# Kernel tuning notes

Measured on AMD Instinct MI355X. Metric: run time of the kernel, lower is better.

## Reference

```python
import jax, jax.numpy as jnp
import numpy as np

B, H, W, D = 4, 64, 64, 384
M, P = 12, 9
DH = D // M             # 32 head dim
DFF = 3 * D             # 1152 FFN hidden
N = H * W               # 4096 queries (single level)


def setup_inputs():
    key = jax.random.key(0)
    ks = jax.random.split(key, 12)
    g = lambda k, s, sc=0.02: jax.random.normal(k, s, jnp.float32) * sc
    return {
        "x": jax.random.normal(ks[0], (B, D, H, W), jnp.float32),
        "qry_masks": jnp.zeros((B, H, W), jnp.float32),
        "so_w": g(ks[1], (M * P * 2, D)), "so_b": g(ks[2], (M * P * 2,)),
        "aw_w": g(ks[3], (M * P, D)), "aw_b": g(ks[4], (M * P,)),
        "vp_w": g(ks[5], (D, D)), "vp_b": jnp.zeros((D,), jnp.float32),
        "op_w": g(ks[6], (D, D)), "op_b": jnp.zeros((D,), jnp.float32),
        "ln1_g": jnp.ones((D,), jnp.float32), "ln1_b": jnp.zeros((D,), jnp.float32),
        "w1": g(ks[7], (DFF, D)), "w2": g(ks[8], (D, DFF)),
        "ln2_g": jnp.ones((D,), jnp.float32), "ln2_b": jnp.zeros((D,), jnp.float32),
        "level_embed": g(ks[9], (1, D), 1.0),
    }


def _layernorm(x, g, b, eps=1e-5):
    mu = x.mean(-1, keepdims=True)
    v = ((x - mu) ** 2).mean(-1, keepdims=True)
    return (x - mu) * jax.lax.rsqrt(v + eps) * g + b


def _sine_pos(mask):
    # mask: [B,H,W] bool. mmdet SinePositionalEncoding(num_feats=D//2, normalize=True)
    not_mask = (~mask).astype(jnp.float32)
    y = jnp.cumsum(not_mask, 1)
    x = jnp.cumsum(not_mask, 2)
    eps, scale = 1e-6, 2.0 * np.pi
    y = y / (y[:, -1:, :] + eps) * scale
    x = x / (x[:, :, -1:] + eps) * scale
    nf = D // 2
    dim_t = 10000.0 ** (2.0 * (jnp.arange(nf) // 2).astype(jnp.float32) / nf)
    px, py = x[..., None] / dim_t, y[..., None] / dim_t

    def interleave(p):
        return jnp.stack([jnp.sin(p[..., 0::2]), jnp.cos(p[..., 1::2])], -1).reshape(p.shape[:-1] + (nf,))

    return jnp.concatenate([interleave(py), interleave(px)], -1)  # [B,H,W,D]


def _bilinear_gather(v, px, py):
    # v: [B,M,HW,DH]; px,py: [B,M,NP] pixel coords (grid_sample align_corners=False, zero pad)
    x0 = jnp.floor(px); y0 = jnp.floor(py)
    lx, ly = px - x0, py - y0
    x0i, y0i = x0.astype(jnp.int32), y0.astype(jnp.int32)
    out = jnp.zeros(v.shape[:2] + (px.shape[-1], v.shape[-1]), v.dtype)
    for dx, dy, wgt in ((0, 0, (1 - lx) * (1 - ly)), (1, 0, lx * (1 - ly)),
                        (0, 1, (1 - lx) * ly), (1, 1, lx * ly)):
        xi, yi = x0i + dx, y0i + dy
        valid = ((xi >= 0) & (xi < W) & (yi >= 0) & (yi < H)).astype(v.dtype)
        idx = jnp.clip(yi, 0, H - 1) * W + jnp.clip(xi, 0, W - 1)
        g = jnp.take_along_axis(v, idx[..., None], axis=2)  # [B,M,NP,DH]
        out = out + (wgt * valid)[..., None] * g
    return out


def _msdeform_attn(q, value_in, ref, mask_flat,
                   so_w, so_b, aw_w, aw_b, vp_w, vp_b, op_w, op_b):
    value = value_in @ vp_w.T + vp_b                      # [B,N,D]
    value = jnp.where(mask_flat[..., None], 0.0, value)
    so = (q @ so_w.T + so_b).reshape(B, N, M, P, 2)       # single level
    aw = jax.nn.softmax((q @ aw_w.T + aw_b).reshape(B, N, M, P), axis=-1)
    norm = jnp.array([W, H], jnp.float32)
    loc = ref[:, :, None, None, :] + so / norm            # [B,N,M,P,2] in [0,1]
    v = value.reshape(B, N, M, DH).transpose(0, 2, 1, 3)  # [B,M,HW,DH]
    px = (loc[..., 0] * W - 0.5).transpose(0, 2, 1, 3).reshape(B, M, N * P)
    py = (loc[..., 1] * H - 0.5).transpose(0, 2, 1, 3).reshape(B, M, N * P)
    sampled = _bilinear_gather(v, px, py).reshape(B, M, N, P, DH)
    out = jnp.einsum('bmnpd,bnmp->bnmd', sampled, aw).reshape(B, N, D)
    return out @ op_w.T + op_b


def reference(x, qry_masks, so_w, so_b, aw_w, aw_b, vp_w, vp_b, op_w, op_b,
              ln1_g, ln1_b, w1, w2, ln2_g, ln2_b, level_embed):
    mask = (qry_masks == 255.0)                           # [B,H,W] bool
    pos = _sine_pos(mask).reshape(B, N, D) + level_embed[0]
    src = x.reshape(B, D, N).transpose(0, 2, 1)           # [B,N,D]
    mask_flat = mask.reshape(B, N)
    gy, gx = jnp.meshgrid((jnp.arange(H, dtype=jnp.float32) + 0.5) / H,
                          (jnp.arange(W, dtype=jnp.float32) + 0.5) / W, indexing='ij')
    ref = jnp.stack([gx.reshape(-1), gy.reshape(-1)], -1)[None]  # [1,N,2] (x,y)
    q = src
    attn = _msdeform_attn(q + pos, q, ref, mask_flat,
                          so_w, so_b, aw_w, aw_b, vp_w, vp_b, op_w, op_b)
    q = _layernorm(q + attn, ln1_g, ln1_b)
    q = _layernorm(q + jax.nn.relu(q @ w1.T) @ w2.T, ln2_g, ln2_b)
    return q.transpose(0, 2, 1).reshape(B, D, H, W)
```

## Files before the change

kernel.cpp:

```cpp
#include <hip/hip_runtime.h>
#include <math.h>

#define Bc   4
#define Hc   64
#define Wc   64
#define Dc   384
#define Nc   4096
#define Mc   12
#define Pc   9
#define DHc  32
#define DFFc 1152
#define BNc  (Bc*Nc)

typedef __attribute__((ext_vector_type(8))) short short8;
typedef __attribute__((ext_vector_type(4))) float floatx4;

__device__ __forceinline__ ushort f2bf(float f) {
    union { float f; unsigned u; } v; v.f = f;
    unsigned r = v.u + 0x7fffu + ((v.u >> 16) & 1u);
    return (ushort)(r >> 16);
}
__device__ __forceinline__ float bf2f(ushort u) {
    union { unsigned u; float f; } v; v.u = (unsigned)u << 16; return v.f;
}

__device__ __forceinline__ void gload_lds16(const void* g, void* l) {
    __builtin_amdgcn_global_load_lds(
        (const __attribute__((address_space(1))) void*)(uintptr_t)g,
        (__attribute__((address_space(3))) void*)(uintptr_t)l,
        16, 0, 0);
}

#define SOW_N  82944
#define AWW_N  41472
#define VPW_N  147456
#define OPW_N  147456
#define W1_N   442368
#define W2_N   442368
#define WTOT   1304064

__global__ void init_kernel(const float* __restrict__ so_w,
                            const float* __restrict__ aw_w,
                            const float* __restrict__ vp_w,
                            const float* __restrict__ op_w,
                            const float* __restrict__ w1,
                            const float* __restrict__ w2,
                            const float* __restrict__ so_b,
                            const float* __restrict__ aw_b,
                            const float* __restrict__ qmask,
                            ushort* __restrict__ out,
                            float* __restrict__ bias_out,
                            float* __restrict__ cum_y,
                            float* __restrict__ cum_x) {
    int i = blockIdx.x * 256 + threadIdx.x;
    if (i < WTOT) {
        float v;
        int j = i;
        if (j < SOW_N) v = so_w[j];
        else if ((j -= SOW_N) < AWW_N) v = aw_w[j];
        else if ((j -= AWW_N) < VPW_N) v = vp_w[j];
        else if ((j -= VPW_N) < OPW_N) v = op_w[j];
        else if ((j -= OPW_N) < W1_N)  v = w1[j];
        else { j -= W1_N; v = w2[j]; }
        out[i] = f2bf(v);
        return;
    }
    int j = i - WTOT;
    if (j < 384) {
        bias_out[j] = (j < 216) ? so_b[j] : (j < 324 ? aw_b[j - 216] : 0.f);
        return;
    }
    int t = j - 384;
    if (t < Bc * Wc) {
        int b = t / Wc, w = t % Wc;
        float run = 0.f;
        for (int h = 0; h < Hc; ++h) {
            run += (qmask[(b * Hc + h) * Wc + w] == 255.0f) ? 0.f : 1.f;
            cum_y[(b * Hc + h) * Wc + w] = run;
        }
    } else if (t < Bc * Wc + Bc * Hc) {
        int t2 = t - Bc * Wc;
        int b = t2 / Hc, h = t2 % Hc;
        float run = 0.f;
        for (int w = 0; w < Wc; ++w) {
            run += (qmask[(b * Hc + h) * Wc + w] == 255.0f) ? 0.f : 1.f;
            cum_x[(b * Hc + h) * Wc + w] = run;
        }
    }
}

__global__ void transpose_pos_kernel(const float* __restrict__ x,
                                     const float* __restrict__ cum_y,
                                     const float* __restrict__ cum_x,
                                     const float* __restrict__ level_embed,
                                     ushort* __restrict__ src_bf,
                                     ushort* __restrict__ qpos_bf) {
    __shared__ float tile[32][33];
    int b  = blockIdx.z;
    int n0 = blockIdx.x * 32, d0 = blockIdx.y * 32;
    int tx = threadIdx.x, ty = threadIdx.y;
    tile[ty][tx] = x[((size_t)b * Dc + (d0 + ty)) * Nc + (n0 + tx)];
    __syncthreads();
    int n = n0 + ty, d = d0 + tx;
    float v = tile[tx][ty];
    size_t oi = ((size_t)b * Nc + n) * Dc + d;
    src_bf[oi] = f2bf(v);
    int h = n >> 6, w = n & 63;
    const float TWO_PI = 6.28318530717958647692f;
    float vy = cum_y[(b * Hc + h) * Wc + w] /
               (cum_y[(b * Hc + (Hc - 1)) * Wc + w] + 1e-6f) * TWO_PI;
    float vx = cum_x[(b * Hc + h) * Wc + w] /
               (cum_x[(b * Hc + h) * Wc + (Wc - 1)] + 1e-6f) * TWO_PI;
    int   i  = (d < 192) ? d : d - 192;
    float vv = (d < 192) ? vy : vx;
    float e   = (float)(i >> 1) * (2.0f / 192.0f);
    float idt = exp2f(e * -13.28771237954945f);
    float ang = vv * idt;
    float pe  = (i & 1) ? __cosf(ang) : __sinf(ang);
    qpos_bf[oi] = f2bf(v + pe + level_embed[d]);
}

template <int KT>
__device__ __forceinline__ void gemm_core(
        const ushort* __restrict__ A, const ushort* __restrict__ Wt,
        const float* __restrict__ bias,
        float* __restrict__ Cf, ushort* __restrict__ Cb,
        int Nout, int relu, const float* __restrict__ qmask,
        ushort* As, ushort* Bs) {
    constexpr int NCH = KT / 32;
    const int tid  = threadIdx.x;
    const int m0   = blockIdx.x * 128;
    const int n0   = blockIdx.y * 128;
    const int lane = tid & 63;
    const int wv   = tid >> 6;
    const int wr   = (wv >> 1) * 64;
    const int wc   = (wv & 1) * 64;
    const int quad = lane >> 4;
    const int lrow = lane & 15;
    const int srow = wv * 32 + (lane >> 2);
    const int scol = (lane & 3) * 8;

    floatx4 acc[4][4];
    #pragma unroll
    for (int i = 0; i < 4; ++i)
        #pragma unroll
        for (int j = 0; j < 4; ++j)
            acc[i][j] = (floatx4)(0.f);

    #pragma unroll
    for (int s = 0; s < 2; ++s) {
        gload_lds16(A  + (size_t)(m0 + srow + s * 16) * KT + scol,
                    As + wv * 1024 + s * 512);
        gload_lds16(Wt + (size_t)(n0 + srow + s * 16) * KT + scol,
                    Bs + wv * 1024 + s * 512);
    }

    for (int c = 0; c < NCH; ++c) {
        const int cur = c & 1;
        __syncthreads();
        if (c + 1 < NCH) {
            const int k0 = (c + 1) * 32;
            #pragma unroll
            for (int s = 0; s < 2; ++s) {
                gload_lds16(A  + (size_t)(m0 + srow + s * 16) * KT + k0 + scol,
                            As + (cur ^ 1) * 4096 + wv * 1024 + s * 512);
                gload_lds16(Wt + (size_t)(n0 + srow + s * 16) * KT + k0 + scol,
                            Bs + (cur ^ 1) * 4096 + wv * 1024 + s * 512);
            }
        }
        short8 afr[4], bfr[4];
        #pragma unroll
        for (int i = 0; i < 4; ++i)
            afr[i] = *(const short8*)(As + cur * 4096 +
                                      (wr + i * 16 + lrow) * 32 + quad * 8);
        #pragma unroll
        for (int j = 0; j < 4; ++j)
            bfr[j] = *(const short8*)(Bs + cur * 4096 +
                                      (wc + j * 16 + lrow) * 32 + quad * 8);
        #pragma unroll
        for (int i = 0; i < 4; ++i)
            #pragma unroll
            for (int j = 0; j < 4; ++j)
                acc[i][j] = __builtin_amdgcn_mfma_f32_16x16x32_bf16(
                    afr[i], bfr[j], acc[i][j], 0, 0, 0);
    }

    float mz[4][4];
    #pragma unroll
    for (int i = 0; i < 4; ++i)
        #pragma unroll
        for (int r = 0; r < 4; ++r) {
            int row = m0 + wr + i * 16 + quad * 4 + r;
            mz[i][r] = (qmask && qmask[row] == 255.0f) ? 0.f : 1.f;
        }

    #pragma unroll
    for (int i = 0; i < 4; ++i) {
        #pragma unroll
        for (int j = 0; j < 4; ++j) {
            int col = n0 + wc + j * 16 + lrow;
            if (col >= Nout) continue;
            float bsv = bias ? bias[col] : 0.f;
            #pragma unroll
            for (int r = 0; r < 4; ++r) {
                int row = m0 + wr + i * 16 + quad * 4 + r;
                float v = acc[i][j][r] + bsv;
                if (relu) v = fmaxf(v, 0.f);
                v *= mz[i][r];
                if (Cf) Cf[(size_t)row * Nout + col] = v;
                if (Cb) Cb[(size_t)row * Nout + col] = f2bf(v);
            }
        }
    }
}

template <int KT>
__global__ __launch_bounds__(256) void gemm_single_kernel(
        const ushort* __restrict__ A, const ushort* __restrict__ Wt,
        const float* __restrict__ bias,
        float* __restrict__ Cf, ushort* __restrict__ Cb,
        int Nout, int relu, const float* __restrict__ qmask) {
    __shared__ ushort As[2 * 128 * 32];
    __shared__ ushort Bs[2 * 128 * 32];
    gemm_core<KT>(A, Wt, bias, Cf, Cb, Nout, relu, qmask, As, Bs);
}

__global__ __launch_bounds__(256) void gemm_dual_kernel(
        const ushort* __restrict__ A0, const ushort* __restrict__ W0,
        const float* __restrict__ b0, float* __restrict__ Cf0,
        const ushort* __restrict__ A1, const ushort* __restrict__ W1,
        const float* __restrict__ b1, ushort* __restrict__ Cb1,
        const float* __restrict__ qmask) {
    __shared__ ushort As[2 * 128 * 32];
    __shared__ ushort Bs[2 * 128 * 32];
    if (blockIdx.z == 0)
        gemm_core<384>(A0, W0, b0, Cf0, nullptr, 384, 0, nullptr, As, Bs);
    else
        gemm_core<384>(A1, W1, b1, nullptr, Cb1, 384, 0, qmask, As, Bs);
}

template <int KT, int MODE>
__global__ __launch_bounds__(512, 4) void gemm_fullrow_kernel(
        const ushort* __restrict__ A, const ushort* __restrict__ Wt,
        const float* __restrict__ bias, const void* __restrict__ resid,
        const float* __restrict__ g, const float* __restrict__ beta,
        float* __restrict__ outf, ushort* __restrict__ outb) {
    constexpr int NCH = KT / 32;
    __shared__ ushort smem[26624];
    __shared__ float eps1[8][32], eps2[8][32];
    __shared__ float mu_l[32], rs_l[32];
    ushort* As = smem;
    ushort* Bs = smem + 2048;
    const int tid  = threadIdx.x;
    const int lane = tid & 63;
    const int wv   = tid >> 6;
    const int quad = lane >> 4;
    const int lrow = lane & 15;
    const int m0   = blockIdx.x * 32;
    const int srow = lane >> 2;
    const int scol = (lane & 3) * 8;

    floatx4 acc[2][3];
    #pragma unroll
    for (int i = 0; i < 2; ++i)
        #pragma unroll
        for (int j = 0; j < 3; ++j)
            acc[i][j] = (floatx4)(0.f);

    if (wv < 2)
        gload_lds16(A + (size_t)(m0 + wv * 16 + srow) * KT + scol,
                    As + wv * 512);
    #pragma unroll
    for (int s = 0; s < 3; ++s)
        gload_lds16(Wt + (size_t)(wv * 48 + s * 16 + srow) * KT + scol,
                    Bs + wv * 1536 + s * 512);

    for (int c = 0; c < NCH; ++c) {
        const int cur = c & 1;
        __syncthreads();
        if (c + 1 < NCH) {
            const int k0 = (c + 1) * 32;
            if (wv < 2)
                gload_lds16(A + (size_t)(m0 + wv * 16 + srow) * KT + k0 + scol,
                            As + (cur ^ 1) * 1024 + wv * 512);
            #pragma unroll
            for (int s = 0; s < 3; ++s)
                gload_lds16(Wt + (size_t)(wv * 48 + s * 16 + srow) * KT + k0 + scol,
                            Bs + (cur ^ 1) * 12288 + wv * 1536 + s * 512);
        }
        short8 afr[2], bfr[3];
        #pragma unroll
        for (int i = 0; i < 2; ++i)
            afr[i] = *(const short8*)(As + cur * 1024 +
                                      (i * 16 + lrow) * 32 + quad * 8);
        #pragma unroll
        for (int j = 0; j < 3; ++j)
            bfr[j] = *(const short8*)(Bs + cur * 12288 +
                                      (wv * 48 + j * 16 + lrow) * 32 + quad * 8);
        #pragma unroll
        for (int i = 0; i < 2; ++i)
            #pragma unroll
            for (int j = 0; j < 3; ++j)
                acc[i][j] = __builtin_amdgcn_mfma_f32_16x16x32_bf16(
                    afr[i], bfr[j], acc[i][j], 0, 0, 0);
    }

    float s1[8], s2[8];
    #pragma unroll
    for (int k = 0; k < 8; ++k) { s1[k] = 0.f; s2[k] = 0.f; }
    #pragma unroll
    for (int i = 0; i < 2; ++i) {
        #pragma unroll
        for (int r = 0; r < 4; ++r) {
            int rl = i * 16 + quad * 4 + r;
            #pragma unroll
            for (int j = 0; j < 3; ++j) {
                int col = wv * 48 + j * 16 + lrow;
                float t = acc[i][j][r];
                if (bias) t += bias[col];
                if (MODE == 0)
                    t += bf2f(((const ushort*)resid)[(size_t)(m0 + rl) * Dc + col]);
                else
                    t += ((const float*)resid)[(size_t)(m0 + rl) * Dc + col];
                acc[i][j][r] = t;
                s1[i * 4 + r] += t;
                s2[i * 4 + r] += t * t;
            }
        }
    }
    #pragma unroll
    for (int mm = 1; mm < 16; mm <<= 1) {
        #pragma unroll
        for (int k = 0; k < 8; ++k) {
            s1[k] += __shfl_xor(s1[k], mm);
            s2[k] += __shfl_xor(s2[k], mm);
        }
    }
    if (lrow == 0) {
        #pragma unroll
        for (int i = 0; i < 2; ++i)
            #pragma unroll
            for (int r = 0; r < 4; ++r) {
                int rl = i * 16 + quad * 4 + r;
                eps1[wv][rl] = s1[i * 4 + r];
                eps2[wv][rl] = s2[i * 4 + r];
            }
    }
    __syncthreads();
    if (tid < 32) {
        float a1 = 0.f, a2 = 0.f;
        #pragma unroll
        for (int w = 0; w < 8; ++w) { a1 += eps1[w][tid]; a2 += eps2[w][tid]; }
        float mu  = a1 * (1.0f / Dc);
        float var = a2 * (1.0f / Dc) - mu * mu;
        mu_l[tid] = mu;
        rs_l[tid] = rsqrtf(var + 1e-5f);
    }
    __syncthreads();

    #pragma unroll
    for (int i = 0; i < 2; ++i) {
        #pragma unroll
        for (int r = 0; r < 4; ++r) {
            int rl = i * 16 + quad * 4 + r;
            float mu = mu_l[rl], rs = rs_l[rl];
            #pragma unroll
            for (int j = 0; j < 3; ++j) {
                int col = wv * 48 + j * 16 + lrow;
                acc[i][j][r] = (acc[i][j][r] - mu) * rs * g[col] + beta[col];
            }
        }
    }

    if (MODE == 0) {
        #pragma unroll
        for (int i = 0; i < 2; ++i)
            #pragma unroll
            for (int j = 0; j < 3; ++j) {
                int col = wv * 48 + j * 16 + lrow;
                #pragma unroll
                for (int r = 0; r < 4; ++r) {
                    int rl = i * 16 + quad * 4 + r;
                    float v = acc[i][j][r];
                    outf[(size_t)(m0 + rl) * Dc + col] = v;
                    outb[(size_t)(m0 + rl) * Dc + col] = f2bf(v);
                }
            }
    } else {
        float* tile = (float*)smem;
        const int b   = m0 >> 12;
        const int n0r = m0 & 4095;
        #pragma unroll
        for (int gp = 0; gp < 2; ++gp) {
            __syncthreads();
            if ((wv >> 2) == gp) {
                int cbase = (wv & 3) * 48;
                #pragma unroll
                for (int i = 0; i < 2; ++i)
                    #pragma unroll
                    for (int j = 0; j < 3; ++j) {
                        int c = cbase + j * 16 + lrow;
                        #pragma unroll
                        for (int r = 0; r < 4; ++r) {
                            int rl = i * 16 + quad * 4 + r;
                            tile[rl * 193 + c] = acc[i][j][r];
                        }
                    }
            }
            __syncthreads();
            const int row = tid & 31;
            const int cp  = tid >> 5;
            #pragma unroll
            for (int it = 0; it < 12; ++it) {
                int c = it * 16 + cp;
                outf[((size_t)(b * Dc + gp * 192 + c)) * Nc + n0r + row] =
                    tile[row * 193 + c];
            }
        }
    }
}

__global__ __launch_bounds__(256) void deform_attn_kernel(
        const ushort* __restrict__ value_bf, const float* __restrict__ soaw,
        ushort* __restrict__ out) {
    int bid   = blockIdx.x;
    int slice = bid % 48;
    int h     = bid / 48;
    int m  = slice % Mc;
    int b  = slice / Mc;
    int w  = threadIdx.x >> 2;
    int l4 = threadIdx.x & 3;
    int n  = (h << 6) | w;
    int bn = b * Nc + n;
    const float* sop = soaw + (size_t)bn * 384 + m * 18;
    const float* lgt = soaw + (size_t)bn * 384 + 216 + m * Pc;
    float awv[Pc];
    float mx = lgt[0];
    #pragma unroll
    for (int i = 1; i < Pc; ++i) mx = fmaxf(mx, lgt[i]);
    float ssum = 0.f;
    #pragma unroll
    for (int i = 0; i < Pc; ++i) { awv[i] = __expf(lgt[i] - mx); ssum += awv[i]; }
    float sinv = 1.f / ssum;
    const ushort* vb = value_bf + ((size_t)b * Nc) * Dc + m * DHc + l4 * 8;
    float acc[8] = {0.f, 0.f, 0.f, 0.f, 0.f, 0.f, 0.f, 0.f};
    #pragma unroll
    for (int p = 0; p < Pc; ++p) {
        float2 so2 = *(const float2*)(sop + p * 2);
        float px = (float)w + so2.x;
        float py = (float)h + so2.y;
        float x0f = floorf(px), y0f = floorf(py);
        float lx = px - x0f, ly = py - y0f;
        int x0 = (int)x0f, y0 = (int)y0f;
        int x1 = x0 + 1,  y1 = y0 + 1;
        float a = awv[p] * sinv;
        float w00 = (1.f - lx) * (1.f - ly) * a;
        float w01 = lx * (1.f - ly) * a;
        float w10 = (1.f - lx) * ly * a;
        float w11 = lx * ly * a;
        bool bx0 = (unsigned)x0 < 64u, bx1 = (unsigned)x1 < 64u;
        bool by0 = (unsigned)y0 < 64u, by1 = (unsigned)y1 < 64u;
        w00 = (bx0 && by0) ? w00 : 0.f;
        w01 = (bx1 && by0) ? w01 : 0.f;
        w10 = (bx0 && by1) ? w10 : 0.f;
        w11 = (bx1 && by1) ? w11 : 0.f;
        int cx0 = min(max(x0, 0), 63), cx1 = min(max(x1, 0), 63);
        int cy0 = min(max(y0, 0), 63), cy1 = min(max(y1, 0), 63);
        uint4 q00 = *(const uint4*)(vb + (size_t)(cy0 * 64 + cx0) * Dc);
        uint4 q01 = *(const uint4*)(vb + (size_t)(cy0 * 64 + cx1) * Dc);
        uint4 q10 = *(const uint4*)(vb + (size_t)(cy1 * 64 + cx0) * Dc);
        uint4 q11 = *(const uint4*)(vb + (size_t)(cy1 * 64 + cx1) * Dc);
        union { unsigned u; float f; } t;
        #define ACC2(word, wg, k)                                   \
            t.u = (word) << 16;         acc[k]     += (wg) * t.f;   \
            t.u = (word) & 0xffff0000u; acc[k + 1] += (wg) * t.f;
        #define ACC8(q, wg) \
            ACC2((q).x, wg, 0) ACC2((q).y, wg, 2) ACC2((q).z, wg, 4) ACC2((q).w, wg, 6)
        ACC8(q00, w00) ACC8(q01, w01) ACC8(q10, w10) ACC8(q11, w11)
        #undef ACC8
        #undef ACC2
    }
    short8 o;
    #pragma unroll
    for (int k = 0; k < 8; ++k) o[k] = (short)f2bf(acc[k]);
    *(short8*)(out + (size_t)bn * Dc + m * DHc + l4 * 8) = o;
}

extern "C" void kernel_launch(void* const* d_in, const int* in_sizes, int n_in,
                              void* d_out, int out_size, void* d_ws, size_t ws_size,
                              hipStream_t stream) {
    (void)in_sizes; (void)n_in; (void)out_size; (void)ws_size;
    const float* x      = (const float*)d_in[0];
    const float* qmask  = (const float*)d_in[1];
    const float* so_w   = (const float*)d_in[2];
    const float* so_b   = (const float*)d_in[3];
    const float* aw_w   = (const float*)d_in[4];
    const float* aw_b   = (const float*)d_in[5];
    const float* vp_w   = (const float*)d_in[6];
    const float* vp_b   = (const float*)d_in[7];
    const float* op_w   = (const float*)d_in[8];
    const float* op_b   = (const float*)d_in[9];
    const float* ln1_g  = (const float*)d_in[10];
    const float* ln1_b  = (const float*)d_in[11];
    const float* w1     = (const float*)d_in[12];
    const float* w2     = (const float*)d_in[13];
    const float* ln2_g  = (const float*)d_in[14];
    const float* ln2_b  = (const float*)d_in[15];
    const float* lvl    = (const float*)d_in[16];
    float* out = (float*)d_out;

    float*  ws       = (float*)d_ws;
    float*  q1_f     = ws;
    ushort* src_bf   = (ushort*)(q1_f + 6291456);
    ushort* qpos_bf  = src_bf + 6291456;
    ushort* value_bf = qpos_bf + 6291456;
    ushort* hbuf_bf  = value_bf + 6291456;
    float*  soaw_f   = (float*)hbuf_bf;
    ushort* wbuf     = hbuf_bf + 18874368;
    float*  soaw_bias= (float*)(wbuf + 1304064);
    float*  cum_y    = soaw_bias + 384;
    float*  cum_x    = cum_y + 16384;

    const ushort* soaw_wb = wbuf;
    const ushort* vp_wb = soaw_wb + SOW_N + AWW_N;
    const ushort* op_wb = vp_wb + VPW_N;
    const ushort* w1_b  = op_wb + OPW_N;
    const ushort* w2_b  = w1_b + W1_N;

    init_kernel<<<(WTOT + 384 + 512 + 255) / 256, 256, 0, stream>>>(
        so_w, aw_w, vp_w, op_w, w1, w2, so_b, aw_b, qmask,
        wbuf, soaw_bias, cum_y, cum_x);
    transpose_pos_kernel<<<dim3(Nc / 32, Dc / 32, Bc), dim3(32, 32), 0, stream>>>(
        x, cum_y, cum_x, lvl, src_bf, qpos_bf);
    gemm_dual_kernel<<<dim3(BNc / 128, 3, 2), 256, 0, stream>>>(
        qpos_bf, soaw_wb, soaw_bias, soaw_f,
        src_bf, vp_wb, vp_b, value_bf, qmask);
    deform_attn_kernel<<<3072, 256, 0, stream>>>(
        value_bf, soaw_f, qpos_bf);
    gemm_fullrow_kernel<384, 0><<<BNc / 32, 512, 0, stream>>>(
        qpos_bf, op_wb, op_b, src_bf, ln1_g, ln1_b, q1_f, qpos_bf);
    gemm_single_kernel<384><<<dim3(BNc / 128, 9), 256, 0, stream>>>(
        qpos_bf, w1_b, nullptr, nullptr, hbuf_bf, DFFc, 1, nullptr);
    gemm_fullrow_kernel<1152, 1><<<BNc / 32, 512, 0, stream>>>(
        hbuf_bf, w2_b, nullptr, q1_f, ln2_g, ln2_b, out, nullptr);
}
```

Baseline: 278.6 us.

## Drop LDS staging in full-row GEMM, load MFMA fragments from global, 64-row tiles

The fused GEMM+LayerNorm kernel no longer stages A and W tiles through double-buffered LDS with barriers. Each wave now reads its MFMA fragments straight from global memory, relying on the cache. Blocks grow to 1024 threads covering 64 rows, with two row-halves of 8 waves each, and the LN reduction and transposed output staging are adjusted to match. This removes LDS traffic and per-chunk syncs, but each wave issues more redundant global loads and there is no software prefetch.

```diff
diff --git a/kernel.cpp b/kernel.cpp
--- a/kernel.cpp
+++ b/kernel.cpp
@@ -240,25 +240,26 @@
 }
 
 template <int KT, int MODE>
-__global__ __launch_bounds__(512, 4) void gemm_fullrow_kernel(
+__global__ __launch_bounds__(1024, 4) void gemm_fullrow_kernel(
         const ushort* __restrict__ A, const ushort* __restrict__ Wt,
         const float* __restrict__ bias, const void* __restrict__ resid,
         const float* __restrict__ g, const float* __restrict__ beta,
         float* __restrict__ outf, ushort* __restrict__ outb) {
     constexpr int NCH = KT / 32;
-    __shared__ ushort smem[26624];
-    __shared__ float eps1[8][32], eps2[8][32];
-    __shared__ float mu_l[32], rs_l[32];
-    ushort* As = smem;
-    ushort* Bs = smem + 2048;
+    __shared__ float tile[(MODE == 1) ? 6208 : 4];
+    __shared__ float eps1[16][64], eps2[16][64];
+    __shared__ float mu_l[64], rs_l[64];
     const int tid  = threadIdx.x;
     const int lane = tid & 63;
     const int wv   = tid >> 6;
+    const int rh   = wv >> 3;
+    const int cg   = wv & 7;
     const int quad = lane >> 4;
     const int lrow = lane & 15;
-    const int m0   = blockIdx.x * 32;
-    const int srow = lane >> 2;
-    const int scol = (lane & 3) * 8;
+    const int m0   = blockIdx.x * 64;
+
+    const ushort* abase = A  + (size_t)(m0 + rh * 32 + lrow) * KT + quad * 8;
+    const ushort* wbase = Wt + (size_t)(cg * 48 + lrow) * KT + quad * 8;
 
     floatx4 acc[2][3];
     #pragma unroll
@@ -267,36 +268,15 @@
         for (int j = 0; j < 3; ++j)
             acc[i][j] = (floatx4)(0.f);
 
-    if (wv < 2)
-        gload_lds16(A + (size_t)(m0 + wv * 16 + srow) * KT + scol,
-                    As + wv * 512);
-    #pragma unroll
-    for (int s = 0; s < 3; ++s)
-        gload_lds16(Wt + (size_t)(wv * 48 + s * 16 + srow) * KT + scol,
-                    Bs + wv * 1536 + s * 512);
-
+    #pragma unroll 2
     for (int c = 0; c < NCH; ++c) {
-        const int cur = c & 1;
-        __syncthreads();
-        if (c + 1 < NCH) {
-            const int k0 = (c + 1) * 32;
-            if (wv < 2)
-                gload_lds16(A + (size_t)(m0 + wv * 16 + srow) * KT + k0 + scol,
-                            As + (cur ^ 1) * 1024 + wv * 512);
-            #pragma unroll
-            for (int s = 0; s < 3; ++s)
-                gload_lds16(Wt + (size_t)(wv * 48 + s * 16 + srow) * KT + k0 + scol,
-                            Bs + (cur ^ 1) * 12288 + wv * 1536 + s * 512);
-        }
         short8 afr[2], bfr[3];
         #pragma unroll
         for (int i = 0; i < 2; ++i)
-            afr[i] = *(const short8*)(As + cur * 1024 +
-                                      (i * 16 + lrow) * 32 + quad * 8);
+            afr[i] = *(const short8*)(abase + (size_t)i * 16 * KT + c * 32);
         #pragma unroll
         for (int j = 0; j < 3; ++j)
-            bfr[j] = *(const short8*)(Bs + cur * 12288 +
-                                      (wv * 48 + j * 16 + lrow) * 32 + quad * 8);
+            bfr[j] = *(const short8*)(wbase + (size_t)j * 16 * KT + c * 32);
         #pragma unroll
         for (int i = 0; i < 2; ++i)
             #pragma unroll
@@ -312,10 +292,10 @@
     for (int i = 0; i < 2; ++i) {
         #pragma unroll
         for (int r = 0; r < 4; ++r) {
-            int rl = i * 16 + quad * 4 + r;
+            int rl = rh * 32 + i * 16 + quad * 4 + r;
             #pragma unroll
             for (int j = 0; j < 3; ++j) {
-                int col = wv * 48 + j * 16 + lrow;
+                int col = cg * 48 + j * 16 + lrow;
                 float t = acc[i][j][r];
                 if (bias) t += bias[col];
                 if (MODE == 0)
@@ -341,16 +321,20 @@
         for (int i = 0; i < 2; ++i)
             #pragma unroll
             for (int r = 0; r < 4; ++r) {
-                int rl = i * 16 + quad * 4 + r;
+                int rl = rh * 32 + i * 16 + quad * 4 + r;
                 eps1[wv][rl] = s1[i * 4 + r];
                 eps2[wv][rl] = s2[i * 4 + r];
             }
     }
     __syncthreads();
-    if (tid < 32) {
+    if (tid < 64) {
+        const int trh = tid >> 5;
         float a1 = 0.f, a2 = 0.f;
         #pragma unroll
-        for (int w = 0; w < 8; ++w) { a1 += eps1[w][tid]; a2 += eps2[w][tid]; }
+        for (int w = 0; w < 8; ++w) {
+            a1 += eps1[trh * 8 + w][tid];
+            a2 += eps2[trh * 8 + w][tid];
+        }
         float mu  = a1 * (1.0f / Dc);
         float var = a2 * (1.0f / Dc) - mu * mu;
         mu_l[tid] = mu;
@@ -362,11 +346,11 @@
     for (int i = 0; i < 2; ++i) {
         #pragma unroll
         for (int r = 0; r < 4; ++r) {
-            int rl = i * 16 + quad * 4 + r;
+            int rl = rh * 32 + i * 16 + quad * 4 + r;
             float mu = mu_l[rl], rs = rs_l[rl];
             #pragma unroll
             for (int j = 0; j < 3; ++j) {
-                int col = wv * 48 + j * 16 + lrow;
+                int col = cg * 48 + j * 16 + lrow;
                 acc[i][j][r] = (acc[i][j][r] - mu) * rs * g[col] + beta[col];
             }
         }
@@ -377,44 +361,43 @@
         for (int i = 0; i < 2; ++i)
             #pragma unroll
             for (int j = 0; j < 3; ++j) {
-                int col = wv * 48 + j * 16 + lrow;
+                int col = cg * 48 + j * 16 + lrow;
                 #pragma unroll
                 for (int r = 0; r < 4; ++r) {
-                    int rl = i * 16 + quad * 4 + r;
+                    int rl = rh * 32 + i * 16 + quad * 4 + r;
                     float v = acc[i][j][r];
                     outf[(size_t)(m0 + rl) * Dc + col] = v;
                     outb[(size_t)(m0 + rl) * Dc + col] = f2bf(v);
                 }
             }
     } else {
-        float* tile = (float*)smem;
         const int b   = m0 >> 12;
         const int n0r = m0 & 4095;
         #pragma unroll
-        for (int gp = 0; gp < 2; ++gp) {
+        for (int q = 0; q < 4; ++q) {
             __syncthreads();
-            if ((wv >> 2) == gp) {
-                int cbase = (wv & 3) * 48;
+            if ((cg >> 1) == q) {
+                int cb = (cg & 1) * 48;
                 #pragma unroll
                 for (int i = 0; i < 2; ++i)
                     #pragma unroll
                     for (int j = 0; j < 3; ++j) {
-                        int c = cbase + j * 16 + lrow;
+                        int c = cb + j * 16 + lrow;
                         #pragma unroll
                         for (int r = 0; r < 4; ++r) {
-                            int rl = i * 16 + quad * 4 + r;
-                            tile[rl * 193 + c] = acc[i][j][r];
+                            int rl = rh * 32 + i * 16 + quad * 4 + r;
+                            tile[rl * 97 + c] = acc[i][j][r];
                         }
                     }
             }
             __syncthreads();
-            const int row = tid & 31;
-            const int cp  = tid >> 5;
-            #pragma unroll
-            for (int it = 0; it < 12; ++it) {
+            const int row = tid & 63;
+            const int cp  = tid >> 6;
+            #pragma unroll
+            for (int it = 0; it < 6; ++it) {
                 int c = it * 16 + cp;
-                outf[((size_t)(b * Dc + gp * 192 + c)) * Nc + n0r + row] =
-                    tile[row * 193 + c];
+                outf[((size_t)(b * Dc + q * 96 + c)) * Nc + n0r + row] =
+                    tile[row * 97 + c];
             }
         }
     }
@@ -537,10 +520,10 @@
         src_bf, vp_wb, vp_b, value_bf, qmask);
     deform_attn_kernel<<<3072, 256, 0, stream>>>(
         value_bf, soaw_f, qpos_bf);
-    gemm_fullrow_kernel<384, 0><<<BNc / 32, 512, 0, stream>>>(
+    gemm_fullrow_kernel<384, 0><<<BNc / 64, 1024, 0, stream>>>(
         qpos_bf, op_wb, op_b, src_bf, ln1_g, ln1_b, q1_f, qpos_bf);
     gemm_single_kernel<384><<<dim3(BNc / 128, 9), 256, 0, stream>>>(
         qpos_bf, w1_b, nullptr, nullptr, hbuf_bf, DFFc, 1, nullptr);
-    gemm_fullrow_kernel<1152, 1><<<BNc / 32, 512, 0, stream>>>(
+    gemm_fullrow_kernel<1152, 1><<<BNc / 64, 1024, 0, stream>>>(
         hbuf_bf, w2_b, nullptr, q1_f, ln2_g, ln2_b, out, nullptr);
 }
```

After: 332.0 us. 19.1% more time.
